# Performance work log

Hardware: AMD Instinct MI355X
Metric: run time of the kernel (lower is better)

The kernel has to match this reference:

```python
import jax, jax.numpy as jnp
import numpy as np

B, N, NVT, HS, NZ = 512, 256, 32, 128, 64


def setup_inputs() -> dict:
    key = jax.random.key(0)
    ks = jax.random.split(key, 16)
    node_types = jax.random.randint(ks[0], (B, N), 0, NVT, dtype=jnp.int32)
    node_types = node_types.at[:, 0].set(0)      # START_TYPE
    node_types = node_types.at[:, -1].set(1)     # END_TYPE
    adj = jax.random.randint(ks[1], (B, N, N), 0, 2, dtype=jnp.int32)
    # DAG: edges only u -> v with u < v (strict upper triangular)
    tri = jnp.triu(jnp.ones((N, N), jnp.int32), k=1)
    adj = adj * tri[None, :, :]
    s = 0.05
    p = lambda k, shp: (jax.random.normal(k, shp, jnp.float32) * s)
    return {
        "node_types": node_types,
        "adj": adj,
        "W_ih": p(ks[2], (3 * HS, NVT)),   # grue_forward weight_ih
        "W_hh": p(ks[3], (3 * HS, HS)),    # grue_forward weight_hh
        "b_ih": p(ks[4], (3 * HS,)),
        "b_hh": p(ks[5], (3 * HS,)),
        "Wg": p(ks[6], (HS, NVT)),         # gate_forward linear
        "bg": p(ks[7], (HS,)),
        "Wm": p(ks[8], (HS, NVT)),         # mapper_forward (no bias)
        "W1": p(ks[9], (NZ, HS)),          # fc1 -> mu
        "b1": p(ks[10], (NZ,)),
        "W2": p(ks[11], (NZ, HS)),         # fc2 -> logvar
        "b2": p(ks[12], (NZ,)),
    }


def reference(node_types, adj, W_ih, W_hh, b_ih, b_hh, Wg, bg, Wm, W1, b1, W2, b2):
    hs = Wg.shape[0]
    # one-hot vertex types  [B, N, nvt]
    X = jax.nn.one_hot(node_types, Wg.shape[1], dtype=W_ih.dtype)
    # gated message from each vertex's TYPE (mapper has no bias -> padding contributes 0)
    gated = jax.nn.sigmoid(jnp.einsum('bnv,hv->bnh', X, Wg) + bg) \
            * jnp.einsum('bnv,hv->bnh', X, Wm)                      # [B, N, hs]
    A = adj.astype(gated.dtype)
    # predecessor aggregation: H_v = sum_{u: u->v} gated_u
    Hpre = jnp.einsum('buv,buh->bvh', A, gated)                     # [B, N, hs]
    # torch GRUCell(X_v, Hpre_v), vectorized over all vertices (no recurrence:
    # messages depend only on predecessor types)
    gi = jnp.einsum('bnv,gv->bng', X, W_ih) + b_ih                  # [B, N, 3hs]
    gh = jnp.einsum('bnh,gh->bng', Hpre, W_hh) + b_hh
    r = jax.nn.sigmoid(gi[..., :hs] + gh[..., :hs])
    z = jax.nn.sigmoid(gi[..., hs:2 * hs] + gh[..., hs:2 * hs])
    n = jnp.tanh(gi[..., 2 * hs:] + r * gh[..., 2 * hs:])
    Hv = (1.0 - z) * n + z * Hpre                                   # H_forward, [B, N, hs]
    # graph state: sum over vertices [1, N-1) (start=1, end_offset=1)
    Hg = Hv[:, 1:-1, :].sum(axis=1)                                 # [B, hs]
    mu = Hg @ W1.T + b1
    logvar = Hg @ W2.T + b2
    return (mu, logvar)
```

## Files before the change

### kernel.cpp

```cpp
#include <hip/hip_runtime.h>
#include <hip/hip_bf16.h>

#define HS 128
#define NVT 32
#define NN 256

typedef __attribute__((ext_vector_type(8))) short bf16x8;
typedef __attribute__((ext_vector_type(4))) short s16x4;
typedef __attribute__((ext_vector_type(4))) float f32x4;

#define TABB_OFF 0
#define GIT_OFF  32768
#define HGP_OFF  65536

static __device__ __forceinline__ short f2bs(float f) {
    __hip_bfloat16 h = __float2bfloat16(f);
    short s; __builtin_memcpy(&s, &h, 2);
    return s;
}
static __device__ __forceinline__ float bs2f(short s) {
    __hip_bfloat16 h; __builtin_memcpy(&h, &s, 2);
    return __bfloat162float(h);
}
static __device__ __forceinline__ float sigm(float x) {
    return __builtin_amdgcn_rcpf(1.f + __expf(-x));
}

__global__ void __launch_bounds__(512) build_tables(
    const float* __restrict__ W_ih, const float* __restrict__ W_hh,
    const float* __restrict__ b_ih, const float* __restrict__ b_hh,
    const float* __restrict__ Wg,   const float* __restrict__ bg,
    const float* __restrict__ Wm,
    short* __restrict__ TABB, short* __restrict__ GIT)
{
    __shared__ float G_s[HS];
    const int t = blockIdx.x;
    const int j = threadIdx.x;
    if (j < HS) {
        float x = Wg[j * NVT + t] + bg[j];
        G_s[j] = sigm(x) * Wm[j * NVT + t];
    }
    __syncthreads();
    if (j < 384) {
        float acc = 0.f;
        for (int h = 0; h < HS; ++h) acc += G_s[h] * W_hh[j * HS + h];
        TABB[j * NVT + t] = f2bs(acc);
        float git = W_ih[j * NVT + t] + b_ih[j];
        if (j < 256) git += b_hh[j];
        GIT[t * 512 + (j & 127) * 4 + (j >> 7)] = f2bs(git);
    } else {
        TABB[j * NVT + t] = f2bs(G_s[j - 384]);
    }
}

__global__ void __launch_bounds__(512) dvae_fused(
    const int* __restrict__ node_types, const int* __restrict__ adj,
    const short* __restrict__ TABB, const short* __restrict__ GIT,
    const float* __restrict__ b_hh,
    float* __restrict__ hgpart)
{
    __shared__ int types_s[NN];
    __shared__ unsigned tmask[NVT * 8];
    __shared__ unsigned short cmask16[16 * 128];
    __shared__ unsigned cntA[128 * 20];

    const int bid = blockIdx.x;
    const int b = bid >> 1, vbase = (bid & 1) << 7;
    const int tid = threadIdx.x;
    const int wave = tid >> 6, lane = tid & 63;
    const int quad = lane >> 4, col = lane & 15;

    if (tid < NN) types_s[tid] = node_types[b * NN + tid];

    bf16x8 bfrag[4];
    #pragma unroll
    for (int g = 0; g < 4; ++g) {
        int jb = (g < 3 ? g * 128 : 384) + wave * 16;
        bfrag[g] = *(const bf16x8*)(TABB + (jb + col) * 32 + quad * 8);
    }
    const int h0 = wave * 16 + col;
    const float bhn = b_hh[256 + h0];

    {
        const int cg = tid & 31, rb = tid >> 5;
        const int4* ap = (const int4*)(adj + (size_t)b * NN * NN + rb * 16 * NN + vbase) + cg;
        unsigned m0 = 0, m1 = 0, m2 = 0, m3 = 0;
        #pragma unroll
        for (int j = 0; j < 16; ++j) {
            int4 a = ap[j * (NN / 4)];
            m0 |= ((unsigned)a.x) << j;
            m1 |= ((unsigned)a.y) << j;
            m2 |= ((unsigned)a.z) << j;
            m3 |= ((unsigned)a.w) << j;
        }
        uint2 pk;
        pk.x = m0 | (m1 << 16);
        pk.y = m2 | (m3 << 16);
        *(uint2*)&cmask16[rb * 128 + cg * 4] = pk;
    }
    __syncthreads();

    if (tid < NN) {
        int t = tid >> 3, w8 = tid & 7;
        unsigned mw = 0;
        #pragma unroll
        for (int k = 0; k < 32; ++k)
            mw |= ((unsigned)(types_s[w8 * 32 + k] == t)) << k;
        tmask[tid] = mw;
    }
    __syncthreads();

    {
        const int v = tid & 127, tpg = tid >> 7;
        unsigned cb[8];
        #pragma unroll
        for (int w = 0; w < 8; ++w)
            cb[w] = (unsigned)cmask16[2 * w * 128 + v]
                  | ((unsigned)cmask16[(2 * w + 1) * 128 + v] << 16);
        #pragma unroll
        for (int k = 0; k < 4; ++k) {
            int tp = tpg * 4 + k;
            const uint4* m0p = (const uint4*)&tmask[(2 * tp) * 8];
            const uint4* m1p = (const uint4*)&tmask[(2 * tp + 1) * 8];
            uint4 ma = m0p[0], mb = m0p[1], mc = m1p[0], md = m1p[1];
            unsigned c0 = __popc(cb[0] & ma.x) + __popc(cb[1] & ma.y)
                        + __popc(cb[2] & ma.z) + __popc(cb[3] & ma.w)
                        + __popc(cb[4] & mb.x) + __popc(cb[5] & mb.y)
                        + __popc(cb[6] & mb.z) + __popc(cb[7] & mb.w);
            unsigned c1 = __popc(cb[0] & mc.x) + __popc(cb[1] & mc.y)
                        + __popc(cb[2] & mc.z) + __popc(cb[3] & mc.w)
                        + __popc(cb[4] & md.x) + __popc(cb[5] & md.y)
                        + __popc(cb[6] & md.z) + __popc(cb[7] & md.w);
            unsigned p = (__float_as_uint((float)c0) >> 16)
                       | (__float_as_uint((float)c1) & 0xFFFF0000u);
            cntA[v * 20 + tp] = p;
        }
    }
    __syncthreads();

    float hg = 0.f;
    for (int m = 0; m < 8; ++m) {
        bf16x8 afrag = *(const bf16x8*)(cntA + (m * 16 + col) * 20 + quad * 4);
        f32x4 acc[4];
        #pragma unroll
        for (int g = 0; g < 4; ++g)
            acc[g] = __builtin_amdgcn_mfma_f32_16x16x32_bf16(
                afrag, bfrag[g], (f32x4){0.f, 0.f, 0.f, 0.f}, 0, 0, 0);
        #pragma unroll
        for (int r = 0; r < 4; ++r) {
            int vv = vbase + m * 16 + quad * 4 + r;
            int tv = types_s[vv];
            s16x4 gv = *(const s16x4*)(GIT + tv * 512 + h0 * 4);
            float gir = bs2f(gv[0]);
            float giz = bs2f(gv[1]);
            float gin = bs2f(gv[2]);
            float rr = sigm(gir + acc[0][r]);
            float zz = sigm(giz + acc[1][r]);
            float x2 = gin + rr * (acc[2][r] + bhn);
            float nt = 1.f - 2.f * __builtin_amdgcn_rcpf(1.f + __expf(2.f * x2));
            float msk = (vv >= 1 && vv < NN - 1) ? 1.f : 0.f;
            hg += msk * ((1.f - zz) * nt + zz * acc[3][r]);
        }
    }
    hg += __shfl_xor(hg, 16);
    hg += __shfl_xor(hg, 32);
    if (lane < 16) hgpart[bid * HS + h0] = hg;
}

__global__ void __launch_bounds__(128) dvae_readout(
    const float* __restrict__ hgpart,
    const float* __restrict__ W1, const float* __restrict__ b1,
    const float* __restrict__ W2, const float* __restrict__ b2,
    float* __restrict__ out)
{
    __shared__ float hg_s[HS];
    const int b = blockIdx.x, tid = threadIdx.x;
    hg_s[tid] = hgpart[(2 * b) * HS + tid] + hgpart[(2 * b + 1) * HS + tid];
    __syncthreads();
    const int which = tid >> 6, z = tid & 63;
    const float* W = which ? W2 : W1;
    float acc = which ? b2[z] : b1[z];
    const float4* Wv = (const float4*)(W + z * HS);
    #pragma unroll
    for (int i = 0; i < 32; ++i) {
        float4 ww = Wv[i];
        acc += hg_s[4 * i] * ww.x + hg_s[4 * i + 1] * ww.y
             + hg_s[4 * i + 2] * ww.z + hg_s[4 * i + 3] * ww.w;
    }
    out[which * 32768 + b * 64 + z] = acc;
}

extern "C" void kernel_launch(void* const* d_in, const int* in_sizes, int n_in,
                              void* d_out, int out_size, void* d_ws, size_t ws_size,
                              hipStream_t stream)
{
    const int* node_types = (const int*)d_in[0];
    const int* adj        = (const int*)d_in[1];
    const float* W_ih = (const float*)d_in[2];
    const float* W_hh = (const float*)d_in[3];
    const float* b_ih = (const float*)d_in[4];
    const float* b_hh = (const float*)d_in[5];
    const float* Wg   = (const float*)d_in[6];
    const float* bg   = (const float*)d_in[7];
    const float* Wm   = (const float*)d_in[8];
    const float* W1   = (const float*)d_in[9];
    const float* b1   = (const float*)d_in[10];
    const float* W2   = (const float*)d_in[11];
    const float* b2   = (const float*)d_in[12];

    char* ws = (char*)d_ws;
    short* TABB   = (short*)(ws + TABB_OFF);
    short* GIT    = (short*)(ws + GIT_OFF);
    float* hgpart = (float*)(ws + HGP_OFF);
    float* out    = (float*)d_out;

    build_tables<<<dim3(32), dim3(512), 0, stream>>>(W_ih, W_hh, b_ih, b_hh, Wg, bg, Wm, TABB, GIT);
    dvae_fused<<<dim3(1024), dim3(512), 0, stream>>>(node_types, adj, TABB, GIT, b_hh, hgpart);
    dvae_readout<<<dim3(512), dim3(128), 0, stream>>>(hgpart, W1, b1, W2, b2, out);
}
```

Measured before the change: 236.9 us.

## Split histogram from GRU stage and fuse readout into per-graph GRU kernel

The fused kernel is split in two. The first kernel reads adj and writes predecessor-type counts, packed as bf16, to global workspace. The second kernel runs one block per graph over all 256 vertices, does the MFMA plus GRU step, and computes the mu/logvar readout in place, so the separate readout launch and the hgpart partial sums go away. This decouples the adj-bandwidth-bound stage from the compute stage, at the cost of a global round trip for the count table (about 8 MB) and half as many blocks in the GRU stage.

```diff
diff --git a/kernel.cpp b/kernel.cpp
--- a/kernel.cpp
+++ b/kernel.cpp
@@ -11,7 +11,7 @@
 
 #define TABB_OFF 0
 #define GIT_OFF  32768
-#define HGP_OFF  65536
+#define CNT_OFF  65536
 
 static __device__ __forceinline__ short f2bs(float f) {
     __hip_bfloat16 h = __float2bfloat16(f);
@@ -53,33 +53,19 @@
     }
 }
 
-__global__ void __launch_bounds__(512) dvae_fused(
+__global__ void __launch_bounds__(512) dvae_hist(
     const int* __restrict__ node_types, const int* __restrict__ adj,
-    const short* __restrict__ TABB, const short* __restrict__ GIT,
-    const float* __restrict__ b_hh,
-    float* __restrict__ hgpart)
+    unsigned* __restrict__ cnt)
 {
     __shared__ int types_s[NN];
     __shared__ unsigned tmask[NVT * 8];
     __shared__ unsigned short cmask16[16 * 128];
-    __shared__ unsigned cntA[128 * 20];
 
     const int bid = blockIdx.x;
     const int b = bid >> 1, vbase = (bid & 1) << 7;
     const int tid = threadIdx.x;
-    const int wave = tid >> 6, lane = tid & 63;
-    const int quad = lane >> 4, col = lane & 15;
 
     if (tid < NN) types_s[tid] = node_types[b * NN + tid];
-
-    bf16x8 bfrag[4];
-    #pragma unroll
-    for (int g = 0; g < 4; ++g) {
-        int jb = (g < 3 ? g * 128 : 384) + wave * 16;
-        bfrag[g] = *(const bf16x8*)(TABB + (jb + col) * 32 + quad * 8);
-    }
-    const int h0 = wave * 16 + col;
-    const float bhn = b_hh[256 + h0];
 
     {
         const int cg = tid & 31, rb = tid >> 5;
@@ -117,6 +103,7 @@
         for (int w = 0; w < 8; ++w)
             cb[w] = (unsigned)cmask16[2 * w * 128 + v]
                   | ((unsigned)cmask16[(2 * w + 1) * 128 + v] << 16);
+        unsigned outp[4];
         #pragma unroll
         for (int k = 0; k < 4; ++k) {
             int tp = tpg * 4 + k;
@@ -131,16 +118,45 @@
                         + __popc(cb[2] & mc.z) + __popc(cb[3] & mc.w)
                         + __popc(cb[4] & md.x) + __popc(cb[5] & md.y)
                         + __popc(cb[6] & md.z) + __popc(cb[7] & md.w);
-            unsigned p = (__float_as_uint((float)c0) >> 16)
-                       | (__float_as_uint((float)c1) & 0xFFFF0000u);
-            cntA[v * 20 + tp] = p;
-        }
-    }
-    __syncthreads();
-
+            outp[k] = (__float_as_uint((float)c0) >> 16)
+                    | (__float_as_uint((float)c1) & 0xFFFF0000u);
+        }
+        *(uint4*)(cnt + (size_t)(b * NN + vbase + v) * 16 + tpg * 4) =
+            (uint4){outp[0], outp[1], outp[2], outp[3]};
+    }
+}
+
+__global__ void __launch_bounds__(512) dvae_gru(
+    const int* __restrict__ node_types, const unsigned* __restrict__ cnt,
+    const short* __restrict__ TABB, const short* __restrict__ GIT,
+    const float* __restrict__ b_hh,
+    const float* __restrict__ W1, const float* __restrict__ b1,
+    const float* __restrict__ W2, const float* __restrict__ b2,
+    float* __restrict__ out)
+{
+    __shared__ int types_s[NN];
+    __shared__ float hg_s[HS];
+
+    const int b = blockIdx.x, tid = threadIdx.x;
+    const int wave = tid >> 6, lane = tid & 63;
+    const int quad = lane >> 4, col = lane & 15;
+
+    if (tid < NN) types_s[tid] = node_types[b * NN + tid];
+
+    bf16x8 bfrag[4];
+    #pragma unroll
+    for (int g = 0; g < 4; ++g) {
+        int jb = (g < 3 ? g * 128 : 384) + wave * 16;
+        bfrag[g] = *(const bf16x8*)(TABB + (jb + col) * 32 + quad * 8);
+    }
+    const int h0 = wave * 16 + col;
+    const float bhn = b_hh[256 + h0];
+    __syncthreads();
+
+    const unsigned* cb = cnt + (size_t)b * NN * 16;
     float hg = 0.f;
-    for (int m = 0; m < 8; ++m) {
-        bf16x8 afrag = *(const bf16x8*)(cntA + (m * 16 + col) * 20 + quad * 4);
+    for (int m = 0; m < 16; ++m) {
+        bf16x8 afrag = *(const bf16x8*)(cb + (m * 16 + col) * 16 + quad * 4);
         f32x4 acc[4];
         #pragma unroll
         for (int g = 0; g < 4; ++g)
@@ -148,7 +164,7 @@
                 afrag, bfrag[g], (f32x4){0.f, 0.f, 0.f, 0.f}, 0, 0, 0);
         #pragma unroll
         for (int r = 0; r < 4; ++r) {
-            int vv = vbase + m * 16 + quad * 4 + r;
+            int vv = m * 16 + quad * 4 + r;
             int tv = types_s[vv];
             s16x4 gv = *(const s16x4*)(GIT + tv * 512 + h0 * 4);
             float gir = bs2f(gv[0]);
@@ -164,30 +180,22 @@
     }
     hg += __shfl_xor(hg, 16);
     hg += __shfl_xor(hg, 32);
-    if (lane < 16) hgpart[bid * HS + h0] = hg;
-}
-
-__global__ void __launch_bounds__(128) dvae_readout(
-    const float* __restrict__ hgpart,
-    const float* __restrict__ W1, const float* __restrict__ b1,
-    const float* __restrict__ W2, const float* __restrict__ b2,
-    float* __restrict__ out)
-{
-    __shared__ float hg_s[HS];
-    const int b = blockIdx.x, tid = threadIdx.x;
-    hg_s[tid] = hgpart[(2 * b) * HS + tid] + hgpart[(2 * b + 1) * HS + tid];
-    __syncthreads();
-    const int which = tid >> 6, z = tid & 63;
-    const float* W = which ? W2 : W1;
-    float acc = which ? b2[z] : b1[z];
-    const float4* Wv = (const float4*)(W + z * HS);
-    #pragma unroll
-    for (int i = 0; i < 32; ++i) {
-        float4 ww = Wv[i];
-        acc += hg_s[4 * i] * ww.x + hg_s[4 * i + 1] * ww.y
-             + hg_s[4 * i + 2] * ww.z + hg_s[4 * i + 3] * ww.w;
-    }
-    out[which * 32768 + b * 64 + z] = acc;
+    if (lane < 16) hg_s[h0] = hg;
+    __syncthreads();
+
+    if (tid < 128) {
+        int which = tid >> 6, zz = tid & 63;
+        const float* W = which ? W2 : W1;
+        float acc2 = which ? b2[zz] : b1[zz];
+        const float4* Wv = (const float4*)(W + zz * HS);
+        #pragma unroll
+        for (int i = 0; i < 32; ++i) {
+            float4 ww = Wv[i];
+            acc2 += hg_s[4 * i] * ww.x + hg_s[4 * i + 1] * ww.y
+                  + hg_s[4 * i + 2] * ww.z + hg_s[4 * i + 3] * ww.w;
+        }
+        out[which * 32768 + b * 64 + zz] = acc2;
+    }
 }
 
 extern "C" void kernel_launch(void* const* d_in, const int* in_sizes, int n_in,
@@ -209,12 +217,12 @@
     const float* b2   = (const float*)d_in[12];
 
     char* ws = (char*)d_ws;
-    short* TABB   = (short*)(ws + TABB_OFF);
-    short* GIT    = (short*)(ws + GIT_OFF);
-    float* hgpart = (float*)(ws + HGP_OFF);
-    float* out    = (float*)d_out;
+    short* TABB  = (short*)(ws + TABB_OFF);
+    short* GIT   = (short*)(ws + GIT_OFF);
+    unsigned* CNT = (unsigned*)(ws + CNT_OFF);
+    float* out   = (float*)d_out;
 
     build_tables<<<dim3(32), dim3(512), 0, stream>>>(W_ih, W_hh, b_ih, b_hh, Wg, bg, Wm, TABB, GIT);
-    dvae_fused<<<dim3(1024), dim3(512), 0, stream>>>(node_types, adj, TABB, GIT, b_hh, hgpart);
-    dvae_readout<<<dim3(512), dim3(128), 0, stream>>>(hgpart, W1, b1, W2, b2, out);
-}
+    dvae_hist<<<dim3(1024), dim3(512), 0, stream>>>(node_types, adj, CNT);
+    dvae_gru<<<dim3(512), dim3(512), 0, stream>>>(node_types, CNT, TABB, GIT, b_hh, W1, b1, W2, b2, out);
+}
```

Measured after the change: 246.7 us. +4.1%, slower.
